# Optimization experiments

Measured on AMD Instinct MI355X. Metric: run time of the kernel, lower is better.

The kernel has to match this reference:

```python
import jax, jax.numpy as jnp
import numpy as np

HID, H, D, DFF = 128, 4, 128, 2048   # hidden_dim, nheads, out_feats per head, dim_feedforward
N, E, B = 32768, 524288, 32
EPS = 1e-5
SLOPE = 0.2  # DGL EdgeGATConv negative_slope default


def setup_inputs() -> dict:
    key = jax.random.key(0)
    ks = jax.random.split(key, 16)
    s = 0.05
    return {
        "h": jax.random.normal(ks[0], (N, HID), jnp.float32),
        "e": jax.random.normal(ks[1], (E, 1), jnp.float32),
        "src": jax.random.randint(ks[2], (E,), 0, N, jnp.int32),
        "dst": jax.random.randint(ks[3], (E,), 0, N, jnp.int32),
        "batch_size": B,
        # EdgeGATConv params (fc / fc_edge / res_fc are bias-free in DGL)
        "W_fc": jax.random.normal(ks[4], (HID, H * D), jnp.float32) * s,
        "attn_l": jax.random.normal(ks[5], (H, D), jnp.float32) * s,
        "attn_r": jax.random.normal(ks[6], (H, D), jnp.float32) * s,
        "W_fe": jax.random.normal(ks[7], (1, H * D), jnp.float32) * s,
        "attn_e": jax.random.normal(ks[8], (H, D), jnp.float32) * s,
        "W_res": jax.random.normal(ks[9], (HID, H * D), jnp.float32) * s,
        "gat_bias": jnp.zeros((H * D,), jnp.float32),
        # linear_mha + norms + FFN
        "W_mha": jax.random.normal(ks[10], (H * D, HID), jnp.float32) * s,
        "b_mha": jnp.zeros((HID,), jnp.float32),
        "n1_g": jnp.ones((HID,), jnp.float32),
        "n1_b": jnp.zeros((HID,), jnp.float32),
        "n2_g": jnp.ones((HID,), jnp.float32),
        "n2_b": jnp.zeros((HID,), jnp.float32),
        "W1": jax.random.normal(ks[11], (HID, DFF), jnp.float32) * s,
        "b1": jnp.zeros((DFF,), jnp.float32),
        "W2": jax.random.normal(ks[12], (DFF, HID), jnp.float32) * s,
        "b2": jnp.zeros((HID,), jnp.float32),
    }


def _ln(x, g, b):
    mu = x.mean(-1, keepdims=True)
    var = ((x - mu) ** 2).mean(-1, keepdims=True)
    return (x - mu) * jax.lax.rsqrt(var + EPS) * g + b


def reference(h, e, src, dst, batch_size, W_fc, attn_l, attn_r, W_fe, attn_e,
              W_res, gat_bias, W_mha, b_mha, n1_g, n1_b, n2_g, n2_b,
              W1, b1, W2, b2):
    n = h.shape[0]
    h0 = h
    # --- EdgeGATConv (eval mode: dropouts are identity) ---
    ft = (h @ W_fc).reshape(n, H, D)                         # (N,H,D)
    el = jnp.einsum("nhd,hd->nh", ft, attn_l)                # (N,H)
    er = jnp.einsum("nhd,hd->nh", ft, attn_r)
    fe = (e @ W_fe).reshape(-1, H, D)                        # (E,H,D)
    ee = jnp.einsum("ehd,hd->eh", fe, attn_e)                # (E,H)
    sc = jax.nn.leaky_relu(el[src] + er[dst] + ee, SLOPE)    # (E,H)
    # segment softmax over incoming edges of each dst node
    m = jax.ops.segment_max(sc, dst, num_segments=n)         # (N,H)
    m = jnp.where(jnp.isfinite(m), m, 0.0)                   # empty segments
    w = jnp.exp(sc - m[dst])
    z = jax.ops.segment_sum(w, dst, num_segments=n)
    zd = z[dst]
    alpha = w / jnp.where(zd == 0, 1.0, zd)                  # (E,H)
    msg = ft[src] * alpha[:, :, None]                        # (E,H,D)
    rst = jax.ops.segment_sum(msg, dst, num_segments=n)      # (N,H,D)
    rst = rst + (h0 @ W_res).reshape(n, H, D) + gat_bias.reshape(1, H, D)
    # --- transformer wrapper ---
    x = jax.nn.relu(rst).reshape(n, H * D)
    x = jax.nn.relu(x @ W_mha + b_mha)
    x = _ln(h0 + x, n1_g, n1_b)
    x = x.reshape(batch_size, -1, x.shape[1])                # (B, N/B, HID)
    ff = jax.nn.relu(x @ W1 + b1) @ W2 + b2
    return _ln(x + ff, n2_g, n2_b)
```

## Files before the change

### kernel.cpp

```cpp
#include <hip/hip_runtime.h>
#include <hip/hip_bf16.h>

#define N_NODES 32768
#define E_EDGES 524288
#define HIDDIM 128
#define FDIM 512
#define DFF 2048
#define LN_EPS 1e-5f
#define SLOPE 0.2f
#define CAP 64

typedef __bf16 bf16_t;
typedef __bf16 bf16x8 __attribute__((ext_vector_type(8)));
typedef float f32x4 __attribute__((ext_vector_type(4)));
typedef float f32x2 __attribute__((ext_vector_type(2)));

#define GLD_LDS16(gp, lp) __builtin_amdgcn_global_load_lds( \
    (const __attribute__((address_space(1))) unsigned int*)(gp), \
    (__attribute__((address_space(3))) unsigned int*)(lp), 16, 0, 0)

__device__ inline unsigned char f32_to_e4m3(float v) {
#if __has_builtin(__builtin_amdgcn_cvt_pk_fp8_f32)
    return (unsigned char)(__builtin_amdgcn_cvt_pk_fp8_f32(v, v, 0, false) & 0xff);
#else
    unsigned bits = __float_as_uint(v);
    unsigned sign = (bits >> 24) & 0x80;
    float av = fabsf(v);
    if (av >= 448.f) return (unsigned char)(sign | 0x7E);
    int e = (int)((bits >> 23) & 0xFF) - 127;
    if (e < -6) { int n = (int)rintf(av * 512.f); return (unsigned char)(sign | n); }
    float ulp = exp2f((float)(e - 3));
    int n = (int)rintf(av / ulp);
    if (n == 16) { e += 1; n = 8; }
    return (unsigned char)(sign | ((e + 7) << 3) | (n - 8));
#endif
}
template<bool HI>
__device__ inline f32x2 e4m3x2_to_f32(unsigned u) {
#if __has_builtin(__builtin_amdgcn_cvt_pk_f32_fp8)
    return __builtin_amdgcn_cvt_pk_f32_fp8(u, HI);
#else
    f32x2 r;
    unsigned b0 = HI ? ((u >> 16) & 0xff) : (u & 0xff);
    unsigned b1 = HI ? ((u >> 24) & 0xff) : ((u >> 8) & 0xff);
    unsigned bs[2] = {b0, b1};
    for (int i = 0; i < 2; ++i) {
        unsigned b = bs[i];
        float s = (b & 0x80) ? -1.f : 1.f;
        int e = (b >> 3) & 15, m = b & 7;
        float v = e ? (8 + m) * exp2f((float)(e - 10)) : m * exp2f(-9.f);
        r[i] = s * v;
    }
    return r;
#endif
}

__device__ inline void pack_range(const float* __restrict__ B, bf16_t* __restrict__ out,
                                  int id, int N) {
    const int g = id / N, n = id % N;
    union { bf16_t b[8]; uint4 u; } pk;
#pragma unroll
    for (int j = 0; j < 8; ++j) pk.b[j] = (bf16_t)B[(size_t)(g * 8 + j) * N + n];
    *(uint4*)(out + (size_t)id * 8) = pk.u;
}

__global__ __launch_bounds__(256) void prep_kernel(const float* __restrict__ h, bf16_t* __restrict__ hb,
                                                   const float* __restrict__ W_fc, bf16_t* __restrict__ Wfc_p,
                                                   const float* __restrict__ W_res, bf16_t* __restrict__ Wres_p,
                                                   const float* __restrict__ W_mha, bf16_t* __restrict__ Wmha_p,
                                                   const float* __restrict__ W1, bf16_t* __restrict__ W1_p,
                                                   const float* __restrict__ W2, bf16_t* __restrict__ W2_p,
                                                   const float* __restrict__ W_fe, const float* __restrict__ attn_e,
                                                   float* __restrict__ ce) {
    int bid = blockIdx.x;
    const int tid = threadIdx.x;
    if (bid < 4096) {
        const int id = bid * 256 + tid;
        const float4 v = ((const float4*)h)[id];
        union { bf16_t b[4]; uint2 u; } pk;
        pk.b[0] = (bf16_t)v.x; pk.b[1] = (bf16_t)v.y; pk.b[2] = (bf16_t)v.z; pk.b[3] = (bf16_t)v.w;
        *(uint2*)(hb + (size_t)id * 4) = pk.u;
        return;
    }
    bid -= 4096;
    if (bid < 32)  { pack_range(W_fc,  Wfc_p,  bid * 256 + tid, 512);  return; }
    bid -= 32;
    if (bid < 32)  { pack_range(W_res, Wres_p, bid * 256 + tid, 512);  return; }
    bid -= 32;
    if (bid < 32)  { pack_range(W_mha, Wmha_p, bid * 256 + tid, 128);  return; }
    bid -= 32;
    if (bid < 128) { pack_range(W1,    W1_p,   bid * 256 + tid, 2048); return; }
    bid -= 128;
    if (bid < 128) { pack_range(W2,    W2_p,   bid * 256 + tid, 128);  return; }
    if (tid < 128) {
        const float4 w = ((const float4*)W_fe)[tid];
        const float4 a = ((const float4*)attn_e)[tid];
        float p = w.x * a.x + w.y * a.y + w.z * a.z + w.w * a.w;
        for (int off = 16; off; off >>= 1) p += __shfl_down(p, off, 32);
        if ((tid & 31) == 0) ce[tid >> 5] = p;
    }
}

__global__ __launch_bounds__(256, 2) void gemm_ftres(const bf16_t* __restrict__ A,
                                                     const bf16_t* __restrict__ Bf,
                                                     const bf16_t* __restrict__ Brs,
                                                     const float* __restrict__ attn_l,
                                                     const float* __restrict__ attn_r,
                                                     unsigned char* __restrict__ ft8,
                                                     float* __restrict__ el,
                                                     float* __restrict__ er,
                                                     bf16_t* __restrict__ res) {
    __shared__ __align__(16) bf16_t lA[4096];
    __shared__ __align__(16) bf16_t lBf[4096];
    __shared__ __align__(16) bf16_t lBr[4096];
    __shared__ float s_el[2][128], s_er[2][128];
    const int tid = threadIdx.x, lane = tid & 63, wave = tid >> 6;
    const int wm = (wave >> 1) * 64, wn = (wave & 1) * 64;
    const int row0 = blockIdx.y * 128;
    const int head = blockIdx.x, col0 = head * 128;
    const int ko = lane >> 4, rl = lane & 15;
    f32x4 accf[4][4] = {};
    f32x4 accr[4][4] = {};
    const int c0 = tid, c1 = tid + 256;
    const int g0 = c0 >> 7, m0 = c0 & 127;
    const int g1 = c1 >> 7, m1 = c1 & 127;
    for (int k0 = 0; k0 < 128; k0 += 32) {
        __syncthreads();
        GLD_LDS16(A + (size_t)(row0 + m0) * 128 + k0 + g0 * 8, lA + c0 * 8);
        GLD_LDS16(A + (size_t)(row0 + m1) * 128 + k0 + g1 * 8, lA + c1 * 8);
        GLD_LDS16(Bf + ((size_t)(k0 / 8 + g0) * 512 + col0 + m0) * 8, lBf + c0 * 8);
        GLD_LDS16(Bf + ((size_t)(k0 / 8 + g1) * 512 + col0 + m1) * 8, lBf + c1 * 8);
        GLD_LDS16(Brs + ((size_t)(k0 / 8 + g0) * 512 + col0 + m0) * 8, lBr + c0 * 8);
        GLD_LDS16(Brs + ((size_t)(k0 / 8 + g1) * 512 + col0 + m1) * 8, lBr + c1 * 8);
        __syncthreads();
        bf16x8 af[4], bff[4], bfr[4];
#pragma unroll
        for (int i = 0; i < 4; ++i) {
            af[i]  = *(const bf16x8*)&lA[(ko * 128 + wm + i * 16 + rl) * 8];
            bff[i] = *(const bf16x8*)&lBf[(ko * 128 + wn + i * 16 + rl) * 8];
            bfr[i] = *(const bf16x8*)&lBr[(ko * 128 + wn + i * 16 + rl) * 8];
        }
#pragma unroll
        for (int i = 0; i < 4; ++i)
#pragma unroll
            for (int j = 0; j < 4; ++j) {
                accf[i][j] = __builtin_amdgcn_mfma_f32_16x16x32_bf16(af[i], bff[j], accf[i][j], 0, 0, 0);
                accr[i][j] = __builtin_amdgcn_mfma_f32_16x16x32_bf16(af[i], bfr[j], accr[i][j], 0, 0, 0);
            }
    }
    const int cr = (lane >> 4) * 4, cc = lane & 15;
    float al[4], ar[4];
#pragma unroll
    for (int j = 0; j < 4; ++j) {
        al[j] = attn_l[col0 + wn + j * 16 + cc];
        ar[j] = attn_r[col0 + wn + j * 16 + cc];
    }
#pragma unroll
    for (int i = 0; i < 4; ++i)
#pragma unroll
        for (int r = 0; r < 4; ++r) {
            const int row = row0 + wm + i * 16 + cr + r;
            float pel = 0.f, per = 0.f;
#pragma unroll
            for (int j = 0; j < 4; ++j) {
                const int col = col0 + wn + j * 16 + cc;
                const float v = accf[i][j][r];
                ft8[(size_t)row * 512 + col] = f32_to_e4m3(v);
                res[(size_t)row * 512 + col] = (bf16_t)accr[i][j][r];
                pel += v * al[j];
                per += v * ar[j];
            }
#pragma unroll
            for (int m = 1; m < 16; m <<= 1) {
                pel += __shfl_xor(pel, m);
                per += __shfl_xor(per, m);
            }
            if (cc == 0) {
                s_el[wn >> 6][wm + i * 16 + cr + r] = pel;
                s_er[wn >> 6][wm + i * 16 + cr + r] = per;
            }
        }
    __syncthreads();
    if (tid < 128) {
        el[(size_t)(row0 + tid) * 4 + head] = s_el[0][tid] + s_el[1][tid];
        er[(size_t)(row0 + tid) * 4 + head] = s_er[0][tid] + s_er[1][tid];
    }
}

__global__ __launch_bounds__(256) void gemm_mha_ln(const bf16_t* __restrict__ A,
                                                   const bf16_t* __restrict__ Bp,
                                                   const float* __restrict__ bias,
                                                   const float* __restrict__ h0,
                                                   const float* __restrict__ gamma,
                                                   const float* __restrict__ beta,
                                                   bf16_t* __restrict__ out) {
    __shared__ __align__(16) bf16_t lA[4096];
    __shared__ __align__(16) bf16_t lB[4096];
    __shared__ float s_s1[2][128], s_s2[2][128], s_mu[128], s_rs[128];
    const int tid = threadIdx.x, lane = tid & 63, wave = tid >> 6;
    const int wm = (wave >> 1) * 64, wn = (wave & 1) * 64;
    const int row0 = blockIdx.x * 128;
    const int ko = lane >> 4, rl = lane & 15;
    f32x4 acc[4][4] = {};
    const int c0 = tid, c1 = tid + 256;
    const int g0 = c0 >> 7, m0 = c0 & 127;
    const int g1 = c1 >> 7, m1 = c1 & 127;
    for (int k0 = 0; k0 < 512; k0 += 32) {
        __syncthreads();
        GLD_LDS16(A + (size_t)(row0 + m0) * 512 + k0 + g0 * 8, lA + c0 * 8);
        GLD_LDS16(A + (size_t)(row0 + m1) * 512 + k0 + g1 * 8, lA + c1 * 8);
        GLD_LDS16(Bp + ((size_t)(k0 / 8 + g0) * 128 + m0) * 8, lB + c0 * 8);
        GLD_LDS16(Bp + ((size_t)(k0 / 8 + g1) * 128 + m1) * 8, lB + c1 * 8);
        __syncthreads();
        bf16x8 af[4], bfr[4];
#pragma unroll
        for (int i = 0; i < 4; ++i) {
            af[i]  = *(const bf16x8*)&lA[(ko * 128 + wm + i * 16 + rl) * 8];
            bfr[i] = *(const bf16x8*)&lB[(ko * 128 + wn + i * 16 + rl) * 8];
        }
#pragma unroll
        for (int i = 0; i < 4; ++i)
#pragma unroll
            for (int j = 0; j < 4; ++j)
                acc[i][j] = __builtin_amdgcn_mfma_f32_16x16x32_bf16(af[i], bfr[j], acc[i][j], 0, 0, 0);
    }
    const int cr = (lane >> 4) * 4, cc = lane & 15;
#pragma unroll
    for (int j = 0; j < 4; ++j) {
        const int col = wn + j * 16 + cc;
        const float bb = bias[col];
#pragma unroll
        for (int i = 0; i < 4; ++i)
#pragma unroll
            for (int r = 0; r < 4; ++r) {
                const int row = row0 + wm + i * 16 + cr + r;
                acc[i][j][r] = fmaxf(acc[i][j][r] + bb, 0.f) + h0[(size_t)row * 128 + col];
            }
    }
#pragma unroll
    for (int i = 0; i < 4; ++i)
#pragma unroll
        for (int r = 0; r < 4; ++r) {
            float s1 = 0.f, s2 = 0.f;
#pragma unroll
            for (int j = 0; j < 4; ++j) { const float v = acc[i][j][r]; s1 += v; s2 += v * v; }
#pragma unroll
            for (int m = 1; m < 16; m <<= 1) {
                s1 += __shfl_xor(s1, m);
                s2 += __shfl_xor(s2, m);
            }
            if (cc == 0) {
                s_s1[wn >> 6][wm + i * 16 + cr + r] = s1;
                s_s2[wn >> 6][wm + i * 16 + cr + r] = s2;
            }
        }
    __syncthreads();
    if (tid < 128) {
        const float a = s_s1[0][tid] + s_s1[1][tid];
        const float q = s_s2[0][tid] + s_s2[1][tid];
        const float mu = a * (1.f / 128.f);
        s_mu[tid] = mu;
        s_rs[tid] = rsqrtf(q * (1.f / 128.f) - mu * mu + LN_EPS);
    }
    __syncthreads();
#pragma unroll
    for (int j = 0; j < 4; ++j) {
        const int col = wn + j * 16 + cc;
        const float gg = gamma[col], bb = beta[col];
#pragma unroll
        for (int i = 0; i < 4; ++i)
#pragma unroll
            for (int r = 0; r < 4; ++r) {
                const int rloc = wm + i * 16 + cr + r;
                out[(size_t)(row0 + rloc) * 128 + col] =
                    (bf16_t)((acc[i][j][r] - s_mu[rloc]) * s_rs[rloc] * gg + bb);
            }
    }
}

__global__ __launch_bounds__(512, 2) void ffn_fused(const bf16_t* __restrict__ x3,
                                                    const bf16_t* __restrict__ W1p,
                                                    const float* __restrict__ b1,
                                                    const bf16_t* __restrict__ W2p,
                                                    const float* __restrict__ b2,
                                                    const float* __restrict__ gamma,
                                                    const float* __restrict__ beta,
                                                    float* __restrict__ out) {
    __shared__ __align__(16) bf16_t lW1[3][8192];
    __shared__ __align__(16) bf16_t lW2[3][8192];
    __shared__ __align__(16) bf16_t lY[8192];
    __shared__ float s_s1[2][128], s_s2[2][128], s_mu[128], s_rs[128];
    const int tid = threadIdx.x, lane = tid & 63, wave = tid >> 6;
    const int wr  = (wave >> 1) * 32;
    const int wc1 = (wave & 1) * 32;
    const int wc2 = (wave & 1) * 64;
    const int row0 = blockIdx.x * 128;
    const int ko = lane >> 4, rl = lane & 15;
    const int cr = ko * 4, cc = rl;

    bf16_t* lX = &lW1[0][0];
#pragma unroll
    for (int it = 0; it < 4; ++it) {
        const int c = it * 512 + tid, g = c >> 7, m = c & 127;
        GLD_LDS16(x3 + (size_t)(row0 + m) * 128 + g * 8, lX + c * 8);
    }
    __syncthreads();
    bf16x8 afx[2][4];
#pragma unroll
    for (int i = 0; i < 2; ++i)
#pragma unroll
        for (int kk = 0; kk < 4; ++kk)
            afx[i][kk] = *(const bf16x8*)&lX[((kk * 4 + ko) * 128 + wr + i * 16 + rl) * 8];
    asm volatile("s_waitcnt lgkmcnt(0)" ::: "memory");
    __builtin_amdgcn_s_barrier();
    __builtin_amdgcn_sched_barrier(0);

#pragma unroll
    for (int pc = 0; pc < 2; ++pc) {
#pragma unroll
        for (int it = 0; it < 2; ++it) {
            const int c = it * 512 + tid;
            { const int g = c >> 6, n = c & 63;
              GLD_LDS16(W1p + ((size_t)g * 2048 + pc * 64 + n) * 8, lW1[pc] + c * 8); }
            { const int g = c >> 7, n = c & 127;
              GLD_LDS16(W2p + ((size_t)(pc * 8 + g) * 128 + n) * 8, lW2[pc] + c * 8); }
        }
    }
    asm volatile("s_waitcnt vmcnt(4)" ::: "memory");
    __builtin_amdgcn_s_barrier();
    __builtin_amdgcn_sched_barrier(0);

    f32x4 xacc[2][4] = {};
    for (int ch = 0; ch < 32; ++ch) {
        const int cur = ch % 3;
        const bf16_t* w1c = lW1[cur];
        const bf16_t* w2c = lW2[cur];
        if (ch + 2 < 32) {
            const int nb = (ch + 2) % 3;
#pragma unroll
            for (int it = 0; it < 2; ++it) {
                const int c = it * 512 + tid;
                { const int g = c >> 6, n = c & 63;
                  GLD_LDS16(W1p + ((size_t)g * 2048 + (ch + 2) * 64 + n) * 8, lW1[nb] + c * 8); }
                { const int g = c >> 7, n = c & 127;
                  GLD_LDS16(W2p + ((size_t)((ch + 2) * 8 + g) * 128 + n) * 8, lW2[nb] + c * 8); }
            }
        }
        f32x4 yacc[2][2] = {};
        __builtin_amdgcn_s_setprio(1);
#pragma unroll
        for (int kk = 0; kk < 4; ++kk) {
            bf16x8 bw[2];
#pragma unroll
            for (int jd = 0; jd < 2; ++jd)
                bw[jd] = *(const bf16x8*)&w1c[((kk * 4 + ko) * 64 + wc1 + jd * 16 + rl) * 8];
#pragma unroll
            for (int jd = 0; jd < 2; ++jd)
#pragma unroll
                for (int ir = 0; ir < 2; ++ir)
                    yacc[jd][ir] = __builtin_amdgcn_mfma_f32_16x16x32_bf16(bw[jd], afx[ir][kk], yacc[jd][ir], 0, 0, 0);
        }
        __builtin_amdgcn_s_setprio(0);
#pragma unroll
        for (int jd = 0; jd < 2; ++jd) {
            const int dffb = wc1 + jd * 16 + cr;
            const float4 bb = *(const float4*)(b1 + ch * 64 + dffb);
#pragma unroll
            for (int ir = 0; ir < 2; ++ir) {
                const int rowx = wr + ir * 16 + cc;
                union { bf16_t b[4]; uint2 u; } pk;
                pk.b[0] = (bf16_t)fmaxf(yacc[jd][ir][0] + bb.x, 0.f);
                pk.b[1] = (bf16_t)fmaxf(yacc[jd][ir][1] + bb.y, 0.f);
                pk.b[2] = (bf16_t)fmaxf(yacc[jd][ir][2] + bb.z, 0.f);
                pk.b[3] = (bf16_t)fmaxf(yacc[jd][ir][3] + bb.w, 0.f);
                *(uint2*)&lY[((dffb >> 3) * 128 + rowx) * 8 + (dffb & 7)] = pk.u;
            }
        }
        bf16x8 bw2[2][4];
#pragma unroll
        for (int kk = 0; kk < 2; ++kk)
#pragma unroll
            for (int j = 0; j < 4; ++j)
                bw2[kk][j] = *(const bf16x8*)&w2c[((kk * 4 + ko) * 128 + wc2 + j * 16 + rl) * 8];
        __builtin_amdgcn_sched_barrier(0);
        asm volatile("s_waitcnt lgkmcnt(0)" ::: "memory");
        __builtin_amdgcn_s_barrier();
        __builtin_amdgcn_sched_barrier(0);
        __builtin_amdgcn_s_setprio(1);
#pragma unroll
        for (int kk = 0; kk < 2; ++kk) {
            bf16x8 ay[2];
#pragma unroll
            for (int ir = 0; ir < 2; ++ir)
                ay[ir] = *(const bf16x8*)&lY[((kk * 4 + ko) * 128 + wr + ir * 16 + rl) * 8];
#pragma unroll
            for (int ir = 0; ir < 2; ++ir)
#pragma unroll
                for (int j = 0; j < 4; ++j)
                    xacc[ir][j] = __builtin_amdgcn_mfma_f32_16x16x32_bf16(ay[ir], bw2[kk][j], xacc[ir][j], 0, 0, 0);
        }
        __builtin_amdgcn_s_setprio(0);
        __builtin_amdgcn_sched_barrier(0);
        if (ch < 30) {
            asm volatile("s_waitcnt vmcnt(4)" ::: "memory");
            __builtin_amdgcn_s_barrier();
        } else if (ch < 31) {
            asm volatile("s_waitcnt vmcnt(0)" ::: "memory");
            __builtin_amdgcn_s_barrier();
        }
        __builtin_amdgcn_sched_barrier(0);
    }
#pragma unroll
    for (int j = 0; j < 4; ++j) {
        const int col = wc2 + j * 16 + cc;
        const float bb = b2[col];
#pragma unroll
        for (int ir = 0; ir < 2; ++ir)
#pragma unroll
            for (int r = 0; r < 4; ++r) {
                const int row = wr + ir * 16 + cr + r;
                xacc[ir][j][r] += bb + (float)x3[(size_t)(row0 + row) * 128 + col];
            }
    }
#pragma unroll
    for (int ir = 0; ir < 2; ++ir)
#pragma unroll
        for (int r = 0; r < 4; ++r) {
            float s1 = 0.f, s2 = 0.f;
#pragma unroll
            for (int j = 0; j < 4; ++j) { const float v = xacc[ir][j][r]; s1 += v; s2 += v * v; }
#pragma unroll
            for (int m = 1; m < 16; m <<= 1) {
                s1 += __shfl_xor(s1, m);
                s2 += __shfl_xor(s2, m);
            }
            if (cc == 0) {
                s_s1[wave & 1][wr + ir * 16 + cr + r] = s1;
                s_s2[wave & 1][wr + ir * 16 + cr + r] = s2;
            }
        }
    __syncthreads();
    if (tid < 128) {
        const float a = s_s1[0][tid] + s_s1[1][tid];
        const float q = s_s2[0][tid] + s_s2[1][tid];
        const float mu = a * (1.f / 128.f);
        s_mu[tid] = mu;
        s_rs[tid] = rsqrtf(q * (1.f / 128.f) - mu * mu + LN_EPS);
    }
    __syncthreads();
#pragma unroll
    for (int j = 0; j < 4; ++j) {
        const int col = wc2 + j * 16 + cc;
        const float gg = gamma[col], bb = beta[col];
#pragma unroll
        for (int ir = 0; ir < 2; ++ir)
#pragma unroll
            for (int r = 0; r < 4; ++r) {
                const int rloc = wr + ir * 16 + cr + r;
                out[(size_t)(row0 + rloc) * 128 + col] =
                    (xacc[ir][j][r] - s_mu[rloc]) * s_rs[rloc] * gg + bb;
            }
    }
}

__global__ __launch_bounds__(256) void edge_build(const float* __restrict__ evals,
                                                  const int* __restrict__ src,
                                                  const int* __restrict__ dst,
                                                  const float* __restrict__ el,
                                                  const float* __restrict__ er,
                                                  const float* __restrict__ ce,
                                                  int* __restrict__ cursor,
                                                  int* __restrict__ csr_src,
                                                  float4* __restrict__ csr_w) {
    const int e = blockIdx.x * 256 + threadIdx.x;
    const int s = src[e], d = dst[e];
    const float ev = evals[e];
    const float4 l = *(const float4*)(el + (size_t)s * 4);
    const float4 r = *(const float4*)(er + (size_t)d * 4);
    const float4 c = *(const float4*)ce;
    float4 w;
    {
        float v;
        v = l.x + r.x + ev * c.x; v = v >= 0.f ? v : SLOPE * v; w.x = __expf(v);
        v = l.y + r.y + ev * c.y; v = v >= 0.f ? v : SLOPE * v; w.y = __expf(v);
        v = l.z + r.z + ev * c.z; v = v >= 0.f ? v : SLOPE * v; w.z = __expf(v);
        v = l.w + r.w + ev * c.w; v = v >= 0.f ? v : SLOPE * v; w.w = __expf(v);
    }
    const int pos = atomicAdd(&cursor[d], 1);
    if (pos < CAP) {
        csr_src[(size_t)d * CAP + pos] = s;
        csr_w[(size_t)d * CAP + pos] = w;
    }
}

__global__ __launch_bounds__(128) void aggregate_kernel(const unsigned char* __restrict__ ft8,
                                                        const bf16_t* __restrict__ res,
                                                        const int* __restrict__ cursor,
                                                        const int* __restrict__ csr_src,
                                                        const float4* __restrict__ csr_w,
                                                        const float* __restrict__ gat_bias,
                                                        bf16_t* __restrict__ x1) {
    const int n = blockIdx.x, t = threadIdx.x;
    __shared__ int s_src[CAP];
    __shared__ float s_w[CAP][4];
    const int deg = min(cursor[n], CAP);
    const int ht = t >> 5;
    if (t < deg) {
        s_src[t] = csr_src[(size_t)n * CAP + t];
        *(float4*)s_w[t] = csr_w[(size_t)n * CAP + t];
    }
    __syncthreads();
    float4 acc = {0.f, 0.f, 0.f, 0.f};
    float z = 0.f;
    for (int j = 0; j < deg; ++j) {
        const float w = s_w[j][ht];
        z += w;
        const unsigned u = *(const unsigned*)(ft8 + (size_t)s_src[j] * 512 + t * 4);
        const f32x2 lo = e4m3x2_to_f32<false>(u);
        const f32x2 hi = e4m3x2_to_f32<true>(u);
        acc.x += w * lo[0]; acc.y += w * lo[1];
        acc.z += w * hi[0]; acc.w += w * hi[1];
    }
    const float rz = deg > 0 ? 1.f / z : 0.f;
    const uint2 ur = *(const uint2*)(res + (size_t)n * FDIM + t * 4);
    const float4 gb = ((const float4*)gat_bias)[t];
    union { bf16_t b[4]; uint2 u; } pk;
    pk.b[0] = (bf16_t)fmaxf(acc.x * rz + __uint_as_float(ur.x << 16) + gb.x, 0.f);
    pk.b[1] = (bf16_t)fmaxf(acc.y * rz + __uint_as_float(ur.x & 0xFFFF0000u) + gb.y, 0.f);
    pk.b[2] = (bf16_t)fmaxf(acc.z * rz + __uint_as_float(ur.y << 16) + gb.z, 0.f);
    pk.b[3] = (bf16_t)fmaxf(acc.w * rz + __uint_as_float(ur.y & 0xFFFF0000u) + gb.w, 0.f);
    *(uint2*)(x1 + (size_t)n * FDIM + t * 4) = pk.u;
}

extern "C" void kernel_launch(void* const* d_in, const int* in_sizes, int n_in,
                              void* d_out, int out_size, void* d_ws, size_t ws_size,
                              hipStream_t stream) {
    const float* h        = (const float*)d_in[0];
    const float* evals    = (const float*)d_in[1];
    const int*   src      = (const int*)d_in[2];
    const int*   dst      = (const int*)d_in[3];
    const float* W_fc     = (const float*)d_in[5];
    const float* attn_l   = (const float*)d_in[6];
    const float* attn_r   = (const float*)d_in[7];
    const float* W_fe     = (const float*)d_in[8];
    const float* attn_e   = (const float*)d_in[9];
    const float* W_res    = (const float*)d_in[10];
    const float* gat_bias = (const float*)d_in[11];
    const float* W_mha    = (const float*)d_in[12];
    const float* b_mha    = (const float*)d_in[13];
    const float* n1_g     = (const float*)d_in[14];
    const float* n1_b     = (const float*)d_in[15];
    const float* n2_g     = (const float*)d_in[16];
    const float* n2_b     = (const float*)d_in[17];
    const float* W1       = (const float*)d_in[18];
    const float* b1       = (const float*)d_in[19];
    const float* W2       = (const float*)d_in[20];
    const float* b2       = (const float*)d_in[21];

    char* ws = (char*)d_ws;
    unsigned char* ft8 = (unsigned char*)(ws + 0);
    bf16_t* res     = (bf16_t*)(ws + 16777216ull);
    bf16_t* x1      = (bf16_t*)(ws + 50331648ull);
    float4* csr_w   = (float4*)(ws + 83886080ull);
    int*    csr_src = (int*)   (ws + 117440512ull);
    bf16_t* x3b     = (bf16_t*)(ws + 125829120ull);
    bf16_t* hb      = (bf16_t*)(ws + 134217728ull);
    bf16_t* Wfc_p   = (bf16_t*)(ws + 142606336ull);
    bf16_t* Wres_p  = (bf16_t*)(ws + 142737408ull);
    bf16_t* Wmha_p  = (bf16_t*)(ws + 142868480ull);
    bf16_t* W1_p    = (bf16_t*)(ws + 142999552ull);
    bf16_t* W2_p    = (bf16_t*)(ws + 143523840ull);
    float*  el      = (float*) (ws + 144048128ull);
    float*  er      = (float*) (ws + 144572416ull);
    float*  ce      = (float*) (ws + 145096704ull);
    int*    cursor  = (int*)   (ws + 145096768ull);

    if (ws_size < 146000000ull) return;

    (void)hipMemsetAsync(cursor, 0, 131072, stream);

    prep_kernel<<<4449, 256, 0, stream>>>(h, hb, W_fc, Wfc_p, W_res, Wres_p,
                                          W_mha, Wmha_p, W1, W1_p, W2, W2_p,
                                          W_fe, attn_e, ce);
    gemm_ftres<<<dim3(4, 256), 256, 0, stream>>>(hb, Wfc_p, Wres_p, attn_l, attn_r, ft8, el, er, res);
    edge_build<<<E_EDGES / 256, 256, 0, stream>>>(evals, src, dst, el, er, ce, cursor, csr_src, csr_w);
    aggregate_kernel<<<N_NODES, 128, 0, stream>>>(ft8, res, cursor, csr_src, csr_w, gat_bias, x1);
    gemm_mha_ln<<<256, 256, 0, stream>>>(x1, Wmha_p, b_mha, h, n1_g, n1_b, x3b);
    ffn_fused<<<256, 512, 0, stream>>>(x3b, W1_p, b1, W2_p, b2, n2_g, n2_b, (float*)d_out);
}
```

Before: 287.9 us.

## Software-pipeline FFN so GEMM1 of next chunk overlaps GEMM2 of previous

Restructures the fused FFN chunk loop into a skewed pipeline. Each iteration computes GEMM1 for chunk i into one half of a double-buffered Y tile while GEMM2 consumes chunk i-1's Y from the other half. This removes one of the two block barriers per chunk and gives the scheduler independent MFMA work to interleave. The cost is more LDS: a fourth W2 stage buffer and a second Y buffer. W2 data must now live one iteration longer, and the ring indexing adds complexity.

```diff
diff --git a/kernel.cpp b/kernel.cpp
--- a/kernel.cpp
+++ b/kernel.cpp
@@ -287,8 +287,8 @@
                                                     const float* __restrict__ beta,
                                                     float* __restrict__ out) {
     __shared__ __align__(16) bf16_t lW1[3][8192];
-    __shared__ __align__(16) bf16_t lW2[3][8192];
-    __shared__ __align__(16) bf16_t lY[8192];
+    __shared__ __align__(16) bf16_t lW2[4][8192];
+    __shared__ __align__(16) bf16_t lY[2][8192];
     __shared__ float s_s1[2][128], s_s2[2][128], s_mu[128], s_rs[128];
     const int tid = threadIdx.x, lane = tid & 63, wave = tid >> 6;
     const int wr  = (wave >> 1) * 32;
@@ -315,37 +315,22 @@
     __builtin_amdgcn_s_barrier();
     __builtin_amdgcn_sched_barrier(0);
 
-#pragma unroll
-    for (int pc = 0; pc < 2; ++pc) {
+    auto stage_chunk = [&](int chn, bf16_t* w1d, bf16_t* w2d) {
 #pragma unroll
         for (int it = 0; it < 2; ++it) {
-            const int c = it * 512 + tid;
-            { const int g = c >> 6, n = c & 63;
-              GLD_LDS16(W1p + ((size_t)g * 2048 + pc * 64 + n) * 8, lW1[pc] + c * 8); }
-            { const int g = c >> 7, n = c & 127;
-              GLD_LDS16(W2p + ((size_t)(pc * 8 + g) * 128 + n) * 8, lW2[pc] + c * 8); }
-        }
-    }
-    asm volatile("s_waitcnt vmcnt(4)" ::: "memory");
-    __builtin_amdgcn_s_barrier();
-    __builtin_amdgcn_sched_barrier(0);
+            const int c = it * 512 + tid, g = c >> 6, n = c & 63;
+            GLD_LDS16(W1p + ((size_t)g * 2048 + chn * 64 + n) * 8, w1d + c * 8);
+        }
+#pragma unroll
+        for (int it = 0; it < 2; ++it) {
+            const int c = it * 512 + tid, g = c >> 7, n = c & 127;
+            GLD_LDS16(W2p + ((size_t)(chn * 8 + g) * 128 + n) * 8, w2d + c * 8);
+        }
+    };
 
     f32x4 xacc[2][4] = {};
-    for (int ch = 0; ch < 32; ++ch) {
-        const int cur = ch % 3;
-        const bf16_t* w1c = lW1[cur];
-        const bf16_t* w2c = lW2[cur];
-        if (ch + 2 < 32) {
-            const int nb = (ch + 2) % 3;
-#pragma unroll
-            for (int it = 0; it < 2; ++it) {
-                const int c = it * 512 + tid;
-                { const int g = c >> 6, n = c & 63;
-                  GLD_LDS16(W1p + ((size_t)g * 2048 + (ch + 2) * 64 + n) * 8, lW1[nb] + c * 8); }
-                { const int g = c >> 7, n = c & 127;
-                  GLD_LDS16(W2p + ((size_t)((ch + 2) * 8 + g) * 128 + n) * 8, lW2[nb] + c * 8); }
-            }
-        }
+
+    auto gemm1 = [&](int chn, const bf16_t* w1c, bf16_t* ydst) {
         f32x4 yacc[2][2] = {};
         __builtin_amdgcn_s_setprio(1);
 #pragma unroll
@@ -364,7 +349,7 @@
 #pragma unroll
         for (int jd = 0; jd < 2; ++jd) {
             const int dffb = wc1 + jd * 16 + cr;
-            const float4 bb = *(const float4*)(b1 + ch * 64 + dffb);
+            const float4 bb = *(const float4*)(b1 + chn * 64 + dffb);
 #pragma unroll
             for (int ir = 0; ir < 2; ++ir) {
                 const int rowx = wr + ir * 16 + cc;
@@ -373,43 +358,69 @@
                 pk.b[1] = (bf16_t)fmaxf(yacc[jd][ir][1] + bb.y, 0.f);
                 pk.b[2] = (bf16_t)fmaxf(yacc[jd][ir][2] + bb.z, 0.f);
                 pk.b[3] = (bf16_t)fmaxf(yacc[jd][ir][3] + bb.w, 0.f);
-                *(uint2*)&lY[((dffb >> 3) * 128 + rowx) * 8 + (dffb & 7)] = pk.u;
-            }
-        }
-        bf16x8 bw2[2][4];
-#pragma unroll
-        for (int kk = 0; kk < 2; ++kk)
+                *(uint2*)&ydst[((dffb >> 3) * 128 + rowx) * 8 + (dffb & 7)] = pk.u;
+            }
+        }
+    };
+
+    auto gemm2 = [&](const bf16_t* w2c, const bf16_t* ysrc) {
+        __builtin_amdgcn_s_setprio(1);
+#pragma unroll
+        for (int kk = 0; kk < 2; ++kk) {
+            bf16x8 ay[2], bw2[4];
+#pragma unroll
+            for (int ir = 0; ir < 2; ++ir)
+                ay[ir] = *(const bf16x8*)&ysrc[((kk * 4 + ko) * 128 + wr + ir * 16 + rl) * 8];
 #pragma unroll
             for (int j = 0; j < 4; ++j)
-                bw2[kk][j] = *(const bf16x8*)&w2c[((kk * 4 + ko) * 128 + wc2 + j * 16 + rl) * 8];
+                bw2[j] = *(const bf16x8*)&w2c[((kk * 4 + ko) * 128 + wc2 + j * 16 + rl) * 8];
+#pragma unroll
+            for (int ir = 0; ir < 2; ++ir)
+#pragma unroll
+                for (int j = 0; j < 4; ++j)
+                    xacc[ir][j] = __builtin_amdgcn_mfma_f32_16x16x32_bf16(ay[ir], bw2[j], xacc[ir][j], 0, 0, 0);
+        }
+        __builtin_amdgcn_s_setprio(0);
+    };
+
+#pragma unroll
+    for (int pc = 0; pc < 2; ++pc)
+        stage_chunk(pc, lW1[pc], lW2[pc]);
+    asm volatile("s_waitcnt vmcnt(4)" ::: "memory");
+    __builtin_amdgcn_s_barrier();
+    __builtin_amdgcn_sched_barrier(0);
+
+    stage_chunk(2, lW1[2], lW2[2]);
+    gemm1(0, lW1[0], lY[0]);
+    __builtin_amdgcn_sched_barrier(0);
+    asm volatile("s_waitcnt vmcnt(4) lgkmcnt(0)" ::: "memory");
+    __builtin_amdgcn_s_barrier();
+    __builtin_amdgcn_sched_barrier(0);
+
+    int r1 = 1, s1 = 0, r2 = 0, s2 = 3, p = 1;
+#pragma unroll 1
+    for (int i = 1; i < 32; ++i) {
+        if (i < 30)
+            stage_chunk(i + 2, lW1[s1], lW2[s2]);
+        gemm1(i, lW1[r1], lY[p]);
+        gemm2(lW2[r2], lY[p ^ 1]);
         __builtin_amdgcn_sched_barrier(0);
-        asm volatile("s_waitcnt lgkmcnt(0)" ::: "memory");
+        if (i < 30)
+            asm volatile("s_waitcnt vmcnt(4) lgkmcnt(0)" ::: "memory");
+        else if (i == 30)
+            asm volatile("s_waitcnt vmcnt(2) lgkmcnt(0)" ::: "memory");
+        else
+            asm volatile("s_waitcnt vmcnt(0) lgkmcnt(0)" ::: "memory");
         __builtin_amdgcn_s_barrier();
         __builtin_amdgcn_sched_barrier(0);
-        __builtin_amdgcn_s_setprio(1);
-#pragma unroll
-        for (int kk = 0; kk < 2; ++kk) {
-            bf16x8 ay[2];
-#pragma unroll
-            for (int ir = 0; ir < 2; ++ir)
-                ay[ir] = *(const bf16x8*)&lY[((kk * 4 + ko) * 128 + wr + ir * 16 + rl) * 8];
-#pragma unroll
-            for (int ir = 0; ir < 2; ++ir)
-#pragma unroll
-                for (int j = 0; j < 4; ++j)
-                    xacc[ir][j] = __builtin_amdgcn_mfma_f32_16x16x32_bf16(ay[ir], bw2[kk][j], xacc[ir][j], 0, 0, 0);
-        }
-        __builtin_amdgcn_s_setprio(0);
-        __builtin_amdgcn_sched_barrier(0);
-        if (ch < 30) {
-            asm volatile("s_waitcnt vmcnt(4)" ::: "memory");
-            __builtin_amdgcn_s_barrier();
-        } else if (ch < 31) {
-            asm volatile("s_waitcnt vmcnt(0)" ::: "memory");
-            __builtin_amdgcn_s_barrier();
-        }
-        __builtin_amdgcn_sched_barrier(0);
-    }
+        r1 = (r1 == 2) ? 0 : r1 + 1;
+        s1 = (s1 == 2) ? 0 : s1 + 1;
+        r2 = (r2 == 3) ? 0 : r2 + 1;
+        s2 = (s2 == 3) ? 0 : s2 + 1;
+        p ^= 1;
+    }
+    gemm2(lW2[3], lY[1]);
+
 #pragma unroll
     for (int j = 0; j < 4; ++j) {
         const int col = wc2 + j * 16 + cc;
@@ -426,17 +437,17 @@
     for (int ir = 0; ir < 2; ++ir)
 #pragma unroll
         for (int r = 0; r < 4; ++r) {
-            float s1 = 0.f, s2 = 0.f;
-#pragma unroll
-            for (int j = 0; j < 4; ++j) { const float v = xacc[ir][j][r]; s1 += v; s2 += v * v; }
+            float s1v = 0.f, s2v = 0.f;
+#pragma unroll
+            for (int j = 0; j < 4; ++j) { const float v = xacc[ir][j][r]; s1v += v; s2v += v * v; }
 #pragma unroll
             for (int m = 1; m < 16; m <<= 1) {
-                s1 += __shfl_xor(s1, m);
-                s2 += __shfl_xor(s2, m);
+                s1v += __shfl_xor(s1v, m);
+                s2v += __shfl_xor(s2v, m);
             }
             if (cc == 0) {
-                s_s1[wave & 1][wr + ir * 16 + cr + r] = s1;
-                s_s2[wave & 1][wr + ir * 16 + cr + r] = s2;
+                s_s1[wave & 1][wr + ir * 16 + cr + r] = s1v;
+                s_s2[wave & 1][wr + ir * 16 + cr + r] = s2v;
             }
         }
     __syncthreads();
```

After: 291.1 us. About the same (+1.1%).
